# Optimization experiments

Hardware: AMD Instinct MI355X
Metric: run time of the kernel (lower is better)

The kernel has to match this reference:

```python
import jax, jax.numpy as jnp
import numpy as np

NEG_INF = -1e20

# Dims: s=512 samples, b=2048 background, t=32 trees, f=64 features, h=128 hidden, y=1
S, B, T, F, H, Y = 512, 2048, 32, 64, 128, 1


def setup_inputs() -> dict:
    key = jax.random.key(0)
    ks = jax.random.split(key, 8)
    X = jax.random.normal(ks[0], (S, F), dtype=jnp.float32)
    background_X = jax.random.normal(ks[1], (B, F), dtype=jnp.float32)
    background_y = jax.random.normal(ks[2], (B, Y), dtype=jnp.float32)
    neighbors_hot = jax.random.randint(ks[3], (S, B, T), 0, 2).astype(jnp.bool_)
    # encoder params: Linear(F->H), Tanh, Linear(H->H)  (n_layers=2)
    W1 = jax.random.normal(ks[4], (F, H), dtype=jnp.float32) / np.sqrt(F)
    b1 = jnp.zeros((H,), dtype=jnp.float32)
    W2 = jax.random.normal(ks[5], (H, H), dtype=jnp.float32) / np.sqrt(H)
    b2 = jnp.zeros((H,), dtype=jnp.float32)
    return {"X": X, "background_X": background_X, "background_y": background_y,
            "neighbors_hot": neighbors_hot, "W1": W1, "b1": b1, "W2": W2, "b2": b2}


def reference(X, background_X, background_y, neighbors_hot, W1, b1, W2, b2):
    def encode(x):
        return jnp.tanh(x @ W1 + b1) @ W2 + b2  # Linear-Tanh-Linear

    X_enc = encode(X)                    # (s, h)
    bg_enc = encode(background_X)        # (b, h)
    dots = X_enc @ bg_enc.T              # (s, b)
    # broadcast over trees + mask, softmax over background axis
    scores = jnp.where(neighbors_hot, dots[:, :, None], NEG_INF)  # (s, b, t)
    first_alphas = jax.nn.softmax(scores, axis=1)                 # (s, b, t)
    first_leaf_xs = jnp.einsum('sbt,bf->stf', first_alphas, background_X)
    first_leaf_y = jnp.einsum('sbt,by->sty', first_alphas, background_y)
    return first_leaf_xs, first_leaf_y, first_alphas
```

## Files before the change

kernel.cpp:

```cpp
#include <hip/hip_runtime.h>
#include <hip/hip_bf16.h>

#define NS 512
#define NB 2048
#define NT 32
#define NF 64
#define NH 128

#define OY  ((size_t)NS * NT * NF)
#define OA  (OY + (size_t)NS * NT)

typedef __attribute__((ext_vector_type(8))) short bf16x8;
typedef __attribute__((ext_vector_type(4))) float f32x4;

__device__ __forceinline__ short f2bfs(float x) {
    __hip_bfloat16 h = __float2bfloat16(x);
    return __builtin_bit_cast(short, h);
}
__device__ __forceinline__ unsigned short f2bfu(float x) {
    __hip_bfloat16 h = __float2bfloat16(x);
    return __builtin_bit_cast(unsigned short, h);
}

__global__ void detect_layout_k(const unsigned char* m, int* flag) {
    __shared__ int any1;
    if (threadIdx.x == 0) any1 = 0;
    __syncthreads();
    for (int i = threadIdx.x; i < 4096; i += blockDim.x)
        if ((i & 3) != 0 && m[i] != 0) any1 = 1;
    __syncthreads();
    if (threadIdx.x == 0) *flag = any1;
}

__device__ __forceinline__ unsigned int pack16_bytes(uint4 v) {
    unsigned int r = 0;
    unsigned int xs[4] = {v.x, v.y, v.z, v.w};
    #pragma unroll
    for (int i = 0; i < 4; ++i) {
        unsigned int x = xs[i];
        unsigned int t = (x | ((x & 0x7F7F7F7Fu) + 0x7F7F7F7Fu)) & 0x80808080u;
        t >>= 7;
        unsigned int n = (t | (t >> 7) | (t >> 14) | (t >> 21)) & 0xFu;
        r |= n << (i * 4);
    }
    return r;
}

__global__ __launch_bounds__(256) void pack_mask_k(const void* mask, const int* flag,
                                                   unsigned long long* pm, int nwords) {
    const int w = blockIdx.x * blockDim.x + threadIdx.x;
    if (w >= nwords) return;
    if (*flag) {
        const uint4* mb = (const uint4*)mask;
        uint4 q0 = mb[(size_t)w * 4 + 0];
        uint4 q1 = mb[(size_t)w * 4 + 1];
        uint4 q2 = mb[(size_t)w * 4 + 2];
        uint4 q3 = mb[(size_t)w * 4 + 3];
        unsigned long long r =  (unsigned long long)pack16_bytes(q0)
                             | ((unsigned long long)pack16_bytes(q1) << 16)
                             | ((unsigned long long)pack16_bytes(q2) << 32)
                             | ((unsigned long long)pack16_bytes(q3) << 48);
        pm[w] = r;
    } else {
        const uint4* mi = (const uint4*)mask;
        unsigned long long r = 0;
        #pragma unroll
        for (int i = 0; i < 16; ++i) {
            uint4 v = mi[(size_t)w * 16 + i];
            unsigned int b = (v.x ? 1u : 0u) | (v.y ? 2u : 0u) |
                             (v.z ? 4u : 0u) | (v.w ? 8u : 0u);
            r |= (unsigned long long)b << (i * 4);
        }
        pm[w] = r;
    }
}

__global__ __launch_bounds__(128) void encode_k(const float* __restrict__ X,
        const float* __restrict__ bgX, const float* __restrict__ W1,
        const float* __restrict__ b1, const float* __restrict__ W2,
        const float* __restrict__ b2, float* __restrict__ enc) {
    __shared__ float xr[NF];
    __shared__ float hr[NH];
    const int row = blockIdx.x;
    const int j = threadIdx.x;
    const float* src = (row < NS) ? (X + (size_t)row * NF) : (bgX + (size_t)(row - NS) * NF);
    if (j < NF) xr[j] = src[j];
    __syncthreads();
    float acc = b1[j];
    #pragma unroll 8
    for (int f = 0; f < NF; ++f) acc = fmaf(xr[f], W1[f * NH + j], acc);
    hr[j] = tanhf(acc);
    __syncthreads();
    float acc2 = b2[j];
    #pragma unroll 8
    for (int k = 0; k < NH; ++k) acc2 = fmaf(hr[k], W2[k * NH + j], acc2);
    enc[(size_t)row * NH + j] = acc2;
}

__global__ __launch_bounds__(256) void transpose_bgx_k(const float* __restrict__ bgX,
                                                       unsigned short* __restrict__ bgXT) {
    __shared__ float t_lds[64][65];
    const int b0 = blockIdx.x * 64;
    const int tid = threadIdx.x;
    #pragma unroll
    for (int it = 0; it < 4; ++it) {
        int idx = (it * 256 + tid) * 4;
        int r = idx >> 6, c = idx & 63;
        *(float4*)(&t_lds[r][c]) = *(const float4*)(bgX + (size_t)(b0 + r) * NF + c);
    }
    __syncthreads();
    const int f = tid >> 2, sg = (tid & 3) * 16;
    union { unsigned short u[16]; uint4 q[2]; } pk;
    #pragma unroll
    for (int i = 0; i < 16; ++i) pk.u[i] = f2bfu(t_lds[sg + i][f]);
    uint4* dst = (uint4*)(bgXT + (size_t)f * NB + b0 + sg);
    dst[0] = pk.q[0];
    dst[1] = pk.q[1];
}

__global__ __launch_bounds__(256) void dots_k(const float* __restrict__ Xe,
        const float* __restrict__ Be, float* __restrict__ dots) {
    __shared__ float At[64 * 68];
    __shared__ float Bt[64 * 68];
    const int s0 = blockIdx.y * 64, b0 = blockIdx.x * 64;
    const int tid = threadIdx.x;
    const int ts = tid & 15, tb = tid >> 4;
    float acc[4][4] = {};
    for (int kt = 0; kt < 2; ++kt) {
        __syncthreads();
        #pragma unroll
        for (int it = 0; it < 4; ++it) {
            int idx = tid * 4 + it * 1024;
            int r = idx >> 6, k = idx & 63;
            *(float4*)(&At[r * 68 + k]) = *(const float4*)(Xe + (size_t)(s0 + r) * NH + kt * 64 + k);
            *(float4*)(&Bt[r * 68 + k]) = *(const float4*)(Be + (size_t)(b0 + r) * NH + kt * 64 + k);
        }
        __syncthreads();
        #pragma unroll 4
        for (int k = 0; k < 64; ++k) {
            float a[4], bv[4];
            #pragma unroll
            for (int i = 0; i < 4; ++i) a[i] = At[(ts + 16 * i) * 68 + k];
            #pragma unroll
            for (int jj = 0; jj < 4; ++jj) bv[jj] = Bt[(tb * 4 + jj) * 68 + k];
            #pragma unroll
            for (int i = 0; i < 4; ++i)
                #pragma unroll
                for (int jj = 0; jj < 4; ++jj)
                    acc[i][jj] = fmaf(a[i], bv[jj], acc[i][jj]);
        }
    }
    #pragma unroll
    for (int i = 0; i < 4; ++i) {
        float4 v = make_float4(acc[i][0], acc[i][1], acc[i][2], acc[i][3]);
        *(float4*)(&dots[(size_t)(s0 + ts + 16 * i) * NB + b0 + tb * 4]) = v;
    }
}

__global__ __launch_bounds__(256) void fusedA_k(float* __restrict__ dots,
        const unsigned long long* __restrict__ pmask,
        const unsigned short* __restrict__ bgXT, const float* __restrict__ bgy,
        float* __restrict__ rden_g, float* __restrict__ out) {
    __shared__ float e_lds[NB];
    __shared__ unsigned int mrow[NB];
    __shared__ float ylds[NB];
    __shared__ float red[256];
    __shared__ float red2[256];
    __shared__ float rden_l[NT];
    __shared__ float part[3 * NT * NF];

    const int s = blockIdx.x;
    const int tid = threadIdx.x;
    const int lane = tid & 63, w = tid >> 6;
    const int t = tid & 31, g = tid >> 5;

    float* drow = dots + (size_t)s * NB;
    float4 d0 = *(const float4*)(drow + tid * 8);
    float4 d1 = *(const float4*)(drow + tid * 8 + 4);
    *(float4*)(&e_lds[tid * 8]) = d0;
    *(float4*)(&e_lds[tid * 8 + 4]) = d1;
    red[tid] = fmaxf(fmaxf(fmaxf(d0.x, d0.y), fmaxf(d0.z, d0.w)),
                     fmaxf(fmaxf(d1.x, d1.y), fmaxf(d1.z, d1.w)));
    const uint4* pmrow = (const uint4*)((const unsigned int*)pmask + (size_t)s * NB);
    #pragma unroll
    for (int it = 0; it < 2; ++it)
        *(uint4*)(&mrow[(tid + it * 256) * 4]) = pmrow[tid + it * 256];
    #pragma unroll
    for (int it = 0; it < 2; ++it)
        *(float4*)(&ylds[(tid + it * 256) * 4]) = *(const float4*)(bgy + (tid + it * 256) * 4);
    __syncthreads();
    for (int off = 128; off > 0; off >>= 1) {
        if (tid < off) red[tid] = fmaxf(red[tid], red[tid + off]);
        __syncthreads();
    }
    const float Ms = red[0];
    float ev[8];
    #pragma unroll
    for (int q = 0; q < 8; ++q) {
        ev[q] = __expf(e_lds[tid * 8 + q] - Ms);
        e_lds[tid * 8 + q] = ev[q];
    }
    *(float4*)(drow + tid * 8)     = make_float4(ev[0], ev[1], ev[2], ev[3]);
    *(float4*)(drow + tid * 8 + 4) = make_float4(ev[4], ev[5], ev[6], ev[7]);
    __syncthreads();

    float dsum = 0.f, ysum = 0.f;
    #pragma unroll 4
    for (int i = 0; i < 256; ++i) {
        int b = g * 256 + i;
        float sel = (float)((mrow[b] >> t) & 1u);
        float e = sel * e_lds[b];
        dsum += e;
        ysum = fmaf(e, ylds[b], ysum);
    }
    red[tid] = dsum;
    red2[tid] = ysum;
    __syncthreads();
    if (tid < 32) {
        float den = 0.f, yv = 0.f;
        #pragma unroll
        for (int gg = 0; gg < 8; ++gg) { den += red[gg * 32 + tid]; yv += red2[gg * 32 + tid]; }
        float rd = den > 0.f ? 1.f / den : 0.f;
        rden_l[tid] = rd;
        rden_g[(size_t)s * NT + tid] = rd;
        out[OY + (size_t)s * NT + tid] = yv * rd;
    }
    __syncthreads();

    const int lo = lane & 15, hi = lane >> 4;
    const float rdm0 = rden_l[lo], rdm1 = rden_l[16 + lo];
    f32x4 acc[2][4] = {};
    const unsigned short* bptr = bgXT + (size_t)lo * NB + w * 512 + hi * 8;
    #pragma unroll 2
    for (int ks = 0; ks < 16; ++ks) {
        const int bb = w * 512 + ks * 32 + hi * 8;
        float4 e0 = *(const float4*)(&e_lds[bb]);
        float4 e1 = *(const float4*)(&e_lds[bb + 4]);
        uint4 m0 = *(const uint4*)(&mrow[bb]);
        uint4 m1 = *(const uint4*)(&mrow[bb + 4]);
        float evv[8] = {e0.x, e0.y, e0.z, e0.w, e1.x, e1.y, e1.z, e1.w};
        unsigned int mv[8] = {m0.x, m0.y, m0.z, m0.w, m1.x, m1.y, m1.z, m1.w};
        bf16x8 a0, a1;
        #pragma unroll
        for (int j = 0; j < 8; ++j) {
            unsigned int mj = mv[j] >> lo;
            a0[j] = f2bfs((mj & 1u) ? evv[j] * rdm0 : 0.f);
            a1[j] = f2bfs((mj & 0x10000u) ? evv[j] * rdm1 : 0.f);
        }
        #pragma unroll
        for (int n = 0; n < 4; ++n) {
            uint4 bv = *(const uint4*)(bptr + (size_t)n * 16 * NB + ks * 32);
            bf16x8 bfr = __builtin_bit_cast(bf16x8, bv);
            acc[0][n] = __builtin_amdgcn_mfma_f32_16x16x32_bf16(a0, bfr, acc[0][n], 0, 0, 0);
            acc[1][n] = __builtin_amdgcn_mfma_f32_16x16x32_bf16(a1, bfr, acc[1][n], 0, 0, 0);
        }
    }

    if (w > 0) {
        #pragma unroll
        for (int m = 0; m < 2; ++m)
            #pragma unroll
            for (int n = 0; n < 4; ++n)
                #pragma unroll
                for (int r = 0; r < 4; ++r) {
                    int tt = m * 16 + hi * 4 + r, ff = n * 16 + lo;
                    part[(w - 1) * (NT * NF) + tt * NF + ff] = acc[m][n][r];
                }
    }
    __syncthreads();
    if (w == 0) {
        float* xout = out + (size_t)s * NT * NF;
        #pragma unroll
        for (int m = 0; m < 2; ++m)
            #pragma unroll
            for (int n = 0; n < 4; ++n)
                #pragma unroll
                for (int r = 0; r < 4; ++r) {
                    int tt = m * 16 + hi * 4 + r, ff = n * 16 + lo;
                    int o = tt * NF + ff;
                    xout[o] = acc[m][n][r] + part[o] + part[NT * NF + o] + part[2 * NT * NF + o];
                }
    }
}

__global__ __launch_bounds__(256) void alphas_k(const float* __restrict__ e,
        const unsigned int* __restrict__ pmask32, const float* __restrict__ rden_g,
        float* __restrict__ out) {
    const int tid = threadIdx.x;
    const int blk = blockIdx.x;
    const int s = blk >> 2;
    const int tq = tid & 7;
    const f32x4 rd4 = *(const f32x4*)(rden_g + (size_t)s * NT + tq * 4);
    const float* erow = e + (size_t)s * NB;
    const unsigned int* mr = pmask32 + (size_t)s * NB;
    float* aout = out + OA + (size_t)s * NB * NT;
    const int bbase = (blk & 3) * 512;
    #pragma unroll 4
    for (int it = 0; it < 16; ++it) {
        int fidx = it * 256 + tid;
        int b = bbase + (fidx >> 3);
        float evb = erow[b];
        unsigned int m = mr[b] >> (tq * 4);
        f32x4 v;
        v.x = (m & 1u) ? evb * rd4.x : 0.f;
        v.y = (m & 2u) ? evb * rd4.y : 0.f;
        v.z = (m & 4u) ? evb * rd4.z : 0.f;
        v.w = (m & 8u) ? evb * rd4.w : 0.f;
        __builtin_nontemporal_store(v, (f32x4*)(aout + (size_t)b * NT + tq * 4));
    }
}

extern "C" void kernel_launch(void* const* d_in, const int* in_sizes, int n_in,
                              void* d_out, int out_size, void* d_ws, size_t ws_size,
                              hipStream_t stream) {
    (void)in_sizes; (void)n_in; (void)out_size; (void)ws_size;
    const float* X   = (const float*)d_in[0];
    const float* bgX = (const float*)d_in[1];
    const float* bgy = (const float*)d_in[2];
    const void*  nh  = d_in[3];
    const float* W1  = (const float*)d_in[4];
    const float* b1v = (const float*)d_in[5];
    const float* W2  = (const float*)d_in[6];
    const float* b2v = (const float*)d_in[7];
    float* out = (float*)d_out;
    char* ws = (char*)d_ws;

    int* flag = (int*)ws;
    float* enc = (float*)(ws + 4096);
    float* Xe = enc;
    float* Be = enc + (size_t)NS * NH;
    float* dots = (float*)(ws + 4096 + (size_t)(NS + NB) * NH * 4);
    unsigned long long* pmask = (unsigned long long*)((char*)dots + (size_t)NS * NB * 4);
    unsigned short* bgXT = (unsigned short*)((char*)pmask + (size_t)NS * NB * NT / 64 * 8);
    float* rden_g = (float*)((char*)bgXT + (size_t)NF * NB * 2);

    const int nwords = NS * NB * NT / 64;
    detect_layout_k<<<1, 256, 0, stream>>>((const unsigned char*)nh, flag);
    pack_mask_k<<<nwords / 256, 256, 0, stream>>>(nh, flag, pmask, nwords);
    encode_k<<<NS + NB, 128, 0, stream>>>(X, bgX, W1, b1v, W2, b2v, enc);
    transpose_bgx_k<<<NB / 64, 256, 0, stream>>>(bgX, bgXT);
    dots_k<<<dim3(NB / 64, NS / 64), 256, 0, stream>>>(Xe, Be, dots);
    fusedA_k<<<NS, 256, 0, stream>>>(dots, pmask, bgXT, bgy, rden_g, out);
    alphas_k<<<NS * 4, 256, 0, stream>>>(dots, (const unsigned int*)pmask, rden_g, out);
}
```

Before: 109.8 us.

## Fuse prep kernels and fold softmax denominator and y into MFMA

```diff
diff --git a/kernel.cpp b/kernel.cpp
--- a/kernel.cpp
+++ b/kernel.cpp
@@ -6,6 +6,7 @@
 #define NT 32
 #define NF 64
 #define NH 128
+#define NFX 80
 
 #define OY  ((size_t)NS * NT * NF)
 #define OA  (OY + (size_t)NS * NT)
@@ -13,10 +14,6 @@
 typedef __attribute__((ext_vector_type(8))) short bf16x8;
 typedef __attribute__((ext_vector_type(4))) float f32x4;
 
-__device__ __forceinline__ short f2bfs(float x) {
-    __hip_bfloat16 h = __float2bfloat16(x);
-    return __builtin_bit_cast(short, h);
-}
 __device__ __forceinline__ unsigned short f2bfu(float x) {
     __hip_bfloat16 h = __float2bfloat16(x);
     return __builtin_bit_cast(unsigned short, h);
@@ -46,76 +43,103 @@
     return r;
 }
 
-__global__ __launch_bounds__(256) void pack_mask_k(const void* mask, const int* flag,
-                                                   unsigned long long* pm, int nwords) {
-    const int w = blockIdx.x * blockDim.x + threadIdx.x;
-    if (w >= nwords) return;
-    if (*flag) {
-        const uint4* mb = (const uint4*)mask;
-        uint4 q0 = mb[(size_t)w * 4 + 0];
-        uint4 q1 = mb[(size_t)w * 4 + 1];
-        uint4 q2 = mb[(size_t)w * 4 + 2];
-        uint4 q3 = mb[(size_t)w * 4 + 3];
-        unsigned long long r =  (unsigned long long)pack16_bytes(q0)
-                             | ((unsigned long long)pack16_bytes(q1) << 16)
-                             | ((unsigned long long)pack16_bytes(q2) << 32)
-                             | ((unsigned long long)pack16_bytes(q3) << 48);
-        pm[w] = r;
-    } else {
-        const uint4* mi = (const uint4*)mask;
-        unsigned long long r = 0;
-        #pragma unroll
-        for (int i = 0; i < 16; ++i) {
-            uint4 v = mi[(size_t)w * 16 + i];
-            unsigned int b = (v.x ? 1u : 0u) | (v.y ? 2u : 0u) |
-                             (v.z ? 4u : 0u) | (v.w ? 8u : 0u);
-            r |= (unsigned long long)b << (i * 4);
-        }
-        pm[w] = r;
-    }
-}
-
-__global__ __launch_bounds__(128) void encode_k(const float* __restrict__ X,
-        const float* __restrict__ bgX, const float* __restrict__ W1,
-        const float* __restrict__ b1, const float* __restrict__ W2,
-        const float* __restrict__ b2, float* __restrict__ enc) {
-    __shared__ float xr[NF];
-    __shared__ float hr[NH];
-    const int row = blockIdx.x;
-    const int j = threadIdx.x;
-    const float* src = (row < NS) ? (X + (size_t)row * NF) : (bgX + (size_t)(row - NS) * NF);
-    if (j < NF) xr[j] = src[j];
-    __syncthreads();
-    float acc = b1[j];
-    #pragma unroll 8
-    for (int f = 0; f < NF; ++f) acc = fmaf(xr[f], W1[f * NH + j], acc);
-    hr[j] = tanhf(acc);
-    __syncthreads();
-    float acc2 = b2[j];
-    #pragma unroll 8
-    for (int k = 0; k < NH; ++k) acc2 = fmaf(hr[k], W2[k * NH + j], acc2);
-    enc[(size_t)row * NH + j] = acc2;
-}
-
-__global__ __launch_bounds__(256) void transpose_bgx_k(const float* __restrict__ bgX,
-                                                       unsigned short* __restrict__ bgXT) {
-    __shared__ float t_lds[64][65];
-    const int b0 = blockIdx.x * 64;
+__global__ __launch_bounds__(256) void prep_k(const void* mask, const int* flag,
+        unsigned long long* pm,
+        const float* __restrict__ X, const float* __restrict__ bgX,
+        const float* __restrict__ bgy,
+        const float* __restrict__ W1, const float* __restrict__ b1,
+        const float* __restrict__ W2, const float* __restrict__ b2,
+        float* __restrict__ enc, unsigned short* __restrict__ bgXT2) {
+    __shared__ float cbuf[64 * 65];
+    const int blk = blockIdx.x;
     const int tid = threadIdx.x;
-    #pragma unroll
-    for (int it = 0; it < 4; ++it) {
-        int idx = (it * 256 + tid) * 4;
-        int r = idx >> 6, c = idx & 63;
-        *(float4*)(&t_lds[r][c]) = *(const float4*)(bgX + (size_t)(b0 + r) * NF + c);
-    }
-    __syncthreads();
-    const int f = tid >> 2, sg = (tid & 3) * 16;
-    union { unsigned short u[16]; uint4 q[2]; } pk;
-    #pragma unroll
-    for (int i = 0; i < 16; ++i) pk.u[i] = f2bfu(t_lds[sg + i][f]);
-    uint4* dst = (uint4*)(bgXT + (size_t)f * NB + b0 + sg);
-    dst[0] = pk.q[0];
-    dst[1] = pk.q[1];
+
+    if (blk < 2048) {
+        const int w = blk * 256 + tid;
+        if (*flag) {
+            const uint4* mb = (const uint4*)mask;
+            uint4 q0 = mb[(size_t)w * 4 + 0];
+            uint4 q1 = mb[(size_t)w * 4 + 1];
+            uint4 q2 = mb[(size_t)w * 4 + 2];
+            uint4 q3 = mb[(size_t)w * 4 + 3];
+            unsigned long long r =  (unsigned long long)pack16_bytes(q0)
+                                 | ((unsigned long long)pack16_bytes(q1) << 16)
+                                 | ((unsigned long long)pack16_bytes(q2) << 32)
+                                 | ((unsigned long long)pack16_bytes(q3) << 48);
+            pm[w] = r;
+        } else {
+            const uint4* mi = (const uint4*)mask;
+            unsigned long long r = 0;
+            #pragma unroll
+            for (int i = 0; i < 16; ++i) {
+                uint4 v = mi[(size_t)w * 16 + i];
+                unsigned int b = (v.x ? 1u : 0u) | (v.y ? 2u : 0u) |
+                                 (v.z ? 4u : 0u) | (v.w ? 8u : 0u);
+                r |= (unsigned long long)b << (i * 4);
+            }
+            pm[w] = r;
+        }
+        return;
+    }
+
+    if (blk < 2048 + 320) {
+        const int r0 = (blk - 2048) * 8;
+        float* xr = cbuf;
+        float* hr = cbuf + 512;
+        if (tid < 128) {
+            int r = tid >> 4, c = (tid & 15) * 4;
+            int row = r0 + r;
+            const float* src = (row < NS) ? (X + (size_t)row * NF)
+                                          : (bgX + (size_t)(row - NS) * NF);
+            *(float4*)(&xr[r * 64 + c]) = *(const float4*)(src + c);
+        }
+        __syncthreads();
+        const int j = tid & 127, h = tid >> 7;
+        float a1[4] = {b1[j], b1[j], b1[j], b1[j]};
+        for (int f = 0; f < NF; ++f) {
+            float wv = W1[f * NH + j];
+            #pragma unroll
+            for (int rr = 0; rr < 4; ++rr) a1[rr] = fmaf(xr[(h * 4 + rr) * 64 + f], wv, a1[rr]);
+        }
+        #pragma unroll
+        for (int rr = 0; rr < 4; ++rr) hr[(h * 4 + rr) * 128 + j] = tanhf(a1[rr]);
+        __syncthreads();
+        float a2[4] = {b2[j], b2[j], b2[j], b2[j]};
+        for (int k = 0; k < NH; ++k) {
+            float wv = W2[k * NH + j];
+            #pragma unroll
+            for (int rr = 0; rr < 4; ++rr) a2[rr] = fmaf(hr[(h * 4 + rr) * 128 + k], wv, a2[rr]);
+        }
+        #pragma unroll
+        for (int rr = 0; rr < 4; ++rr) enc[(size_t)(r0 + h * 4 + rr) * NH + j] = a2[rr];
+        return;
+    }
+
+    {
+        const int b0 = (blk - 2368) * 64;
+        float (*t_lds)[65] = (float(*)[65])cbuf;
+        #pragma unroll
+        for (int it = 0; it < 4; ++it) {
+            int idx = (it * 256 + tid) * 4;
+            int r = idx >> 6, c = idx & 63;
+            *(float4*)(&t_lds[r][c]) = *(const float4*)(bgX + (size_t)(b0 + r) * NF + c);
+        }
+        __syncthreads();
+        const int f = tid >> 2, sg = (tid & 3) * 16;
+        union { unsigned short u[16]; uint4 q[2]; } pk;
+        #pragma unroll
+        for (int i = 0; i < 16; ++i) pk.u[i] = f2bfu(t_lds[sg + i][f]);
+        uint4* dst = (uint4*)(bgXT2 + (size_t)f * NB + b0 + sg);
+        dst[0] = pk.q[0];
+        dst[1] = pk.q[1];
+        if (tid < 64) {
+            int b = b0 + tid;
+            bgXT2[(size_t)64 * NB + b] = f2bfu(bgy[b]);
+            bgXT2[(size_t)65 * NB + b] = 0x3F80;
+            #pragma unroll
+            for (int ff = 66; ff < NFX; ++ff) bgXT2[(size_t)ff * NB + b] = 0;
+        }
+    }
 }
 
 __global__ __launch_bounds__(256) void dots_k(const float* __restrict__ Xe,
@@ -159,96 +183,69 @@
 
 __global__ __launch_bounds__(256) void fusedA_k(float* __restrict__ dots,
         const unsigned long long* __restrict__ pmask,
-        const unsigned short* __restrict__ bgXT, const float* __restrict__ bgy,
+        const unsigned short* __restrict__ bgXT2,
         float* __restrict__ rden_g, float* __restrict__ out) {
-    __shared__ float e_lds[NB];
-    __shared__ unsigned int mrow[NB];
-    __shared__ float ylds[NB];
-    __shared__ float red[256];
-    __shared__ float red2[256];
+    __shared__ __align__(16) unsigned int mrow[NB];
+    __shared__ __align__(16) unsigned short e_bf[NB];
+    __shared__ float part[3 * NT * NFX];
+    __shared__ float wmax[4];
     __shared__ float rden_l[NT];
-    __shared__ float part[3 * NT * NF];
+    __shared__ float ytmp[NT];
 
     const int s = blockIdx.x;
     const int tid = threadIdx.x;
     const int lane = tid & 63, w = tid >> 6;
-    const int t = tid & 31, g = tid >> 5;
+    const int lo = lane & 15, hi = lane >> 4;
 
     float* drow = dots + (size_t)s * NB;
     float4 d0 = *(const float4*)(drow + tid * 8);
     float4 d1 = *(const float4*)(drow + tid * 8 + 4);
-    *(float4*)(&e_lds[tid * 8]) = d0;
-    *(float4*)(&e_lds[tid * 8 + 4]) = d1;
-    red[tid] = fmaxf(fmaxf(fmaxf(d0.x, d0.y), fmaxf(d0.z, d0.w)),
-                     fmaxf(fmaxf(d1.x, d1.y), fmaxf(d1.z, d1.w)));
     const uint4* pmrow = (const uint4*)((const unsigned int*)pmask + (size_t)s * NB);
+    *(uint4*)(&mrow[tid * 4]) = pmrow[tid];
+    *(uint4*)(&mrow[(tid + 256) * 4]) = pmrow[tid + 256];
+    float pmax = fmaxf(fmaxf(fmaxf(d0.x, d0.y), fmaxf(d0.z, d0.w)),
+                       fmaxf(fmaxf(d1.x, d1.y), fmaxf(d1.z, d1.w)));
     #pragma unroll
-    for (int it = 0; it < 2; ++it)
-        *(uint4*)(&mrow[(tid + it * 256) * 4]) = pmrow[tid + it * 256];
+    for (int off = 32; off >= 1; off >>= 1)
+        pmax = fmaxf(pmax, __shfl_xor(pmax, off, 64));
+    if (lane == 0) wmax[w] = pmax;
+    __syncthreads();
+    const float Ms = fmaxf(fmaxf(wmax[0], wmax[1]), fmaxf(wmax[2], wmax[3]));
+    float ev[8] = {d0.x, d0.y, d0.z, d0.w, d1.x, d1.y, d1.z, d1.w};
+    union { unsigned short u[8]; uint4 q; } epk;
     #pragma unroll
-    for (int it = 0; it < 2; ++it)
-        *(float4*)(&ylds[(tid + it * 256) * 4]) = *(const float4*)(bgy + (tid + it * 256) * 4);
-    __syncthreads();
-    for (int off = 128; off > 0; off >>= 1) {
-        if (tid < off) red[tid] = fmaxf(red[tid], red[tid + off]);
-        __syncthreads();
-    }
-    const float Ms = red[0];
-    float ev[8];
-    #pragma unroll
-    for (int q = 0; q < 8; ++q) {
-        ev[q] = __expf(e_lds[tid * 8 + q] - Ms);
-        e_lds[tid * 8 + q] = ev[q];
-    }
+    for (int q = 0; q < 8; ++q) { ev[q] = __expf(ev[q] - Ms); epk.u[q] = f2bfu(ev[q]); }
     *(float4*)(drow + tid * 8)     = make_float4(ev[0], ev[1], ev[2], ev[3]);
     *(float4*)(drow + tid * 8 + 4) = make_float4(ev[4], ev[5], ev[6], ev[7]);
-    __syncthreads();
-
-    float dsum = 0.f, ysum = 0.f;
-    #pragma unroll 4
-    for (int i = 0; i < 256; ++i) {
-        int b = g * 256 + i;
-        float sel = (float)((mrow[b] >> t) & 1u);
-        float e = sel * e_lds[b];
-        dsum += e;
-        ysum = fmaf(e, ylds[b], ysum);
-    }
-    red[tid] = dsum;
-    red2[tid] = ysum;
-    __syncthreads();
-    if (tid < 32) {
-        float den = 0.f, yv = 0.f;
-        #pragma unroll
-        for (int gg = 0; gg < 8; ++gg) { den += red[gg * 32 + tid]; yv += red2[gg * 32 + tid]; }
-        float rd = den > 0.f ? 1.f / den : 0.f;
-        rden_l[tid] = rd;
-        rden_g[(size_t)s * NT + tid] = rd;
-        out[OY + (size_t)s * NT + tid] = yv * rd;
-    }
-    __syncthreads();
-
-    const int lo = lane & 15, hi = lane >> 4;
-    const float rdm0 = rden_l[lo], rdm1 = rden_l[16 + lo];
-    f32x4 acc[2][4] = {};
-    const unsigned short* bptr = bgXT + (size_t)lo * NB + w * 512 + hi * 8;
+    *(uint4*)(&e_bf[tid * 8]) = epk.q;
+    __syncthreads();
+
+    f32x4 acc[2][5] = {};
+    const unsigned short* bptr = bgXT2 + (size_t)lo * NB + w * 512 + hi * 8;
     #pragma unroll 2
     for (int ks = 0; ks < 16; ++ks) {
         const int bb = w * 512 + ks * 32 + hi * 8;
-        float4 e0 = *(const float4*)(&e_lds[bb]);
-        float4 e1 = *(const float4*)(&e_lds[bb + 4]);
+        uint4 ew4 = *(const uint4*)(&e_bf[bb]);
         uint4 m0 = *(const uint4*)(&mrow[bb]);
         uint4 m1 = *(const uint4*)(&mrow[bb + 4]);
-        float evv[8] = {e0.x, e0.y, e0.z, e0.w, e1.x, e1.y, e1.z, e1.w};
+        unsigned int ew[4] = {ew4.x, ew4.y, ew4.z, ew4.w};
         unsigned int mv[8] = {m0.x, m0.y, m0.z, m0.w, m1.x, m1.y, m1.z, m1.w};
-        bf16x8 a0, a1;
-        #pragma unroll
-        for (int j = 0; j < 8; ++j) {
-            unsigned int mj = mv[j] >> lo;
-            a0[j] = f2bfs((mj & 1u) ? evv[j] * rdm0 : 0.f);
-            a1[j] = f2bfs((mj & 0x10000u) ? evv[j] * rdm1 : 0.f);
-        }
-        #pragma unroll
-        for (int n = 0; n < 4; ++n) {
+        unsigned int A0[4], A1[4];
+        #pragma unroll
+        for (int p = 0; p < 4; ++p) {
+            unsigned int mlo = mv[2 * p]     >> lo;
+            unsigned int mhi = mv[2 * p + 1] >> lo;
+            unsigned int k0 = ((mlo & 1u)       ? 0x0000FFFFu : 0u) |
+                              ((mhi & 1u)       ? 0xFFFF0000u : 0u);
+            unsigned int k1 = ((mlo & 0x10000u) ? 0x0000FFFFu : 0u) |
+                              ((mhi & 0x10000u) ? 0xFFFF0000u : 0u);
+            A0[p] = ew[p] & k0;
+            A1[p] = ew[p] & k1;
+        }
+        bf16x8 a0 = __builtin_bit_cast(bf16x8, make_uint4(A0[0], A0[1], A0[2], A0[3]));
+        bf16x8 a1 = __builtin_bit_cast(bf16x8, make_uint4(A1[0], A1[1], A1[2], A1[3]));
+        #pragma unroll
+        for (int n = 0; n < 5; ++n) {
             uint4 bv = *(const uint4*)(bptr + (size_t)n * 16 * NB + ks * 32);
             bf16x8 bfr = __builtin_bit_cast(bf16x8, bv);
             acc[0][n] = __builtin_amdgcn_mfma_f32_16x16x32_bf16(a0, bfr, acc[0][n], 0, 0, 0);
@@ -260,26 +257,44 @@
         #pragma unroll
         for (int m = 0; m < 2; ++m)
             #pragma unroll
+            for (int n = 0; n < 5; ++n)
+                #pragma unroll
+                for (int r = 0; r < 4; ++r) {
+                    int t = m * 16 + hi * 4 + r, f = n * 16 + lo;
+                    part[(w - 1) * (NT * NFX) + t * NFX + f] = acc[m][n][r];
+                }
+    }
+    __syncthreads();
+    if (w == 0) {
+        #pragma unroll
+        for (int m = 0; m < 2; ++m)
+            #pragma unroll
+            for (int r = 0; r < 4; ++r) {
+                int t = m * 16 + hi * 4 + r;
+                int o = t * NFX + 64 + lo;
+                float tot = acc[m][4][r] + part[o] + part[NT * NFX + o] + part[2 * NT * NFX + o];
+                if (lo == 0) ytmp[t] = tot;
+                if (lo == 1) rden_l[t] = (tot > 0.f) ? 1.f / tot : 0.f;
+            }
+    }
+    __syncthreads();
+    if (w == 0) {
+        float* xout = out + (size_t)s * NT * NF;
+        #pragma unroll
+        for (int m = 0; m < 2; ++m)
+            #pragma unroll
             for (int n = 0; n < 4; ++n)
                 #pragma unroll
                 for (int r = 0; r < 4; ++r) {
-                    int tt = m * 16 + hi * 4 + r, ff = n * 16 + lo;
-                    part[(w - 1) * (NT * NF) + tt * NF + ff] = acc[m][n][r];
+                    int t = m * 16 + hi * 4 + r, f = n * 16 + lo;
+                    int o = t * NFX + f;
+                    float tot = acc[m][n][r] + part[o] + part[NT * NFX + o] + part[2 * NT * NFX + o];
+                    xout[t * NF + f] = tot * rden_l[t];
                 }
     }
-    __syncthreads();
-    if (w == 0) {
-        float* xout = out + (size_t)s * NT * NF;
-        #pragma unroll
-        for (int m = 0; m < 2; ++m)
-            #pragma unroll
-            for (int n = 0; n < 4; ++n)
-                #pragma unroll
-                for (int r = 0; r < 4; ++r) {
-                    int tt = m * 16 + hi * 4 + r, ff = n * 16 + lo;
-                    int o = tt * NF + ff;
-                    xout[o] = acc[m][n][r] + part[o] + part[NT * NF + o] + part[2 * NT * NF + o];
-                }
+    if (tid < 32) {
+        out[OY + (size_t)s * NT + tid] = ytmp[tid] * rden_l[tid];
+        rden_g[(size_t)s * NT + tid] = rden_l[tid];
     }
 }
 
@@ -327,19 +342,17 @@
 
     int* flag = (int*)ws;
     float* enc = (float*)(ws + 4096);
+    float* rden_g = (float*)(ws + 4096);
     float* Xe = enc;
     float* Be = enc + (size_t)NS * NH;
     float* dots = (float*)(ws + 4096 + (size_t)(NS + NB) * NH * 4);
     unsigned long long* pmask = (unsigned long long*)((char*)dots + (size_t)NS * NB * 4);
-    unsigned short* bgXT = (unsigned short*)((char*)pmask + (size_t)NS * NB * NT / 64 * 8);
-    float* rden_g = (float*)((char*)bgXT + (size_t)NF * NB * 2);
-
-    const int nwords = NS * NB * NT / 64;
+    unsigned short* bgXT2 = (unsigned short*)((char*)pmask + (size_t)NS * NB * NT / 64 * 8);
+
     detect_layout_k<<<1, 256, 0, stream>>>((const unsigned char*)nh, flag);
-    pack_mask_k<<<nwords / 256, 256, 0, stream>>>(nh, flag, pmask, nwords);
-    encode_k<<<NS + NB, 128, 0, stream>>>(X, bgX, W1, b1v, W2, b2v, enc);
-    transpose_bgx_k<<<NB / 64, 256, 0, stream>>>(bgX, bgXT);
+    prep_k<<<2048 + 320 + 32, 256, 0, stream>>>(nh, flag, pmask, X, bgX, bgy,
+                                                W1, b1v, W2, b2v, enc, bgXT2);
     dots_k<<<dim3(NB / 64, NS / 64), 256, 0, stream>>>(Xe, Be, dots);
-    fusedA_k<<<NS, 256, 0, stream>>>(dots, pmask, bgXT, bgy, rden_g, out);
+    fusedA_k<<<NS, 256, 0, stream>>>(dots, pmask, bgXT2, rden_g, out);
     alphas_k<<<NS * 4, 256, 0, stream>>>(dots, (const unsigned int*)pmask, rden_g, out);
 }
```

Result: no change. 111.4 us (+1.5%).
